# Optimization experiments

Hardware: AMD Instinct MI355X
Metric: run time of the kernel (lower is better)

## Reference

```python
import jax, jax.numpy as jnp
import numpy as np

L, D, H, M = 4, 256, 8, 1024  # num_blocks, emb_dim, num_heads, mlp_dim
B, N = 8, 1024
HD = H * D  # per-head dim == emb_dim in this module (hidden_dims = emb_dim*num_heads)


def setup_inputs() -> dict:
    key = jax.random.key(0)
    ks = jax.random.split(key, 6)
    s = 0.02
    return {
        "x": jax.random.normal(ks[0], (B, N, D), jnp.float32),
        "ln1_g": jnp.ones((L, D), jnp.float32),
        "ln1_b": jnp.zeros((L, D), jnp.float32),
        "qkv_w": jax.random.normal(ks[1], (L, D, 3 * HD), jnp.float32) * s,
        "qkv_b": jnp.zeros((L, 3 * HD), jnp.float32),
        "proj_w": jax.random.normal(ks[2], (L, HD, D), jnp.float32) * s,
        "proj_b": jnp.zeros((L, D), jnp.float32),
        "ln2_g": jnp.ones((L, D), jnp.float32),
        "ln2_b": jnp.zeros((L, D), jnp.float32),
        "w1": jax.random.normal(ks[3], (L, D, M), jnp.float32) * s,
        "b1": jnp.zeros((L, M), jnp.float32),
        "w2": jax.random.normal(ks[4], (L, M, D), jnp.float32) * s,
        "b2": jnp.zeros((L, D), jnp.float32),
    }


def _layernorm(x, g, b):
    m = x.mean(-1, keepdims=True)
    v = x.var(-1, keepdims=True)  # torch LayerNorm: biased variance, eps=1e-5
    return (x - m) * jax.lax.rsqrt(v + 1e-5) * g + b


def reference(x, ln1_g, ln1_b, qkv_w, qkv_b, proj_w, proj_b, ln2_g, ln2_b, w1, b1, w2, b2):
    b, n, d = x.shape
    scale = d ** 0.5  # source intends emb_dim**0.5; NOTE: applied AFTER softmax (bug preserved)
    for i in range(L):
        # --- attention residual block (pre-norm) ---
        h = _layernorm(x, ln1_g[i], ln1_b[i])
        qkv = (h @ qkv_w[i] + qkv_b[i]).reshape(b, n, H, d, 3)  # 'b n (h d qkv)'
        q = jnp.transpose(qkv[..., 0], (0, 2, 1, 3))  # [b,H,n,d]
        k = jnp.transpose(qkv[..., 1], (0, 2, 1, 3))
        v = jnp.transpose(qkv[..., 2], (0, 2, 1, 3))
        energy = jnp.einsum('bhqd,bhkd->bhqk', q, k)
        attn = jax.nn.softmax(energy, axis=-1) / scale  # post-softmax scaling as in source
        o = jnp.einsum('bhal,bhlv->bhav', attn, v)
        o = jnp.transpose(o, (0, 2, 1, 3)).reshape(b, n, H * d)
        x = x + (o @ proj_w[i] + proj_b[i])
        # --- MLP residual block (pre-norm) ---
        h = _layernorm(x, ln2_g[i], ln2_b[i])
        h = jax.nn.gelu(h @ w1[i] + b1[i], approximate=False)  # torch nn.GELU default = exact
        x = x + (h @ w2[i] + b2[i])
    return x
```

## Files before the change

kernel.cpp:

```cpp
#include <hip/hip_runtime.h>
#include <cstdint>
#include <cmath>

typedef float f32x4 __attribute__((ext_vector_type(4)));
typedef short s16x8 __attribute__((ext_vector_type(8)));

__device__ __forceinline__ unsigned short f2bf(float f) {
  union { float f; unsigned u; } v; v.f = f;
  unsigned r = v.u + 0x7FFFu + ((v.u >> 16) & 1u);
  return (unsigned short)(r >> 16);
}

__device__ __forceinline__ void async16(const void* g, void* l) {
  __builtin_amdgcn_global_load_lds(
      (const __attribute__((address_space(1))) unsigned int*)g,
      (__attribute__((address_space(3))) unsigned int*)l, 16, 0, 0);
}

#define MFMA(a,b,c) __builtin_amdgcn_mfma_f32_16x16x32_bf16((a),(b),(c),0,0,0)

#define Lb 4
#define Dm 256
#define Hh 8
#define Mm 1024
#define Bb 8
#define Nn 1024
#define ROWS (Bb*Nn)
#define QKVN (3*Hh*Dm)

__global__ __launch_bounds__(256) void ln_kernel(const float* __restrict__ x,
                                                 const float* __restrict__ g,
                                                 const float* __restrict__ b,
                                                 unsigned short* __restrict__ out) {
  int wave = threadIdx.x >> 6, lane = threadIdx.x & 63;
  int row = blockIdx.x * 4 + wave;
  const float4* xr = (const float4*)(x + (size_t)row * Dm);
  float4 v = xr[lane];
  float s = v.x + v.y + v.z + v.w;
  float s2 = v.x*v.x + v.y*v.y + v.z*v.z + v.w*v.w;
  #pragma unroll
  for (int off = 1; off < 64; off <<= 1) {
    s  += __shfl_xor(s,  off);
    s2 += __shfl_xor(s2, off);
  }
  float mean = s * (1.0f/Dm);
  float var  = s2 * (1.0f/Dm) - mean*mean;
  float inv  = rsqrtf(var + 1e-5f);
  float4 gg = ((const float4*)g)[lane];
  float4 bb = ((const float4*)b)[lane];
  ushort4 o;
  o.x = f2bf((v.x-mean)*inv*gg.x + bb.x);
  o.y = f2bf((v.y-mean)*inv*gg.y + bb.y);
  o.z = f2bf((v.z-mean)*inv*gg.z + bb.z);
  o.w = f2bf((v.w-mean)*inv*gg.w + bb.w);
  ((ushort4*)(out + (size_t)row * Dm))[lane] = o;
}

__global__ __launch_bounds__(256) void lncomb_kernel(const float* __restrict__ xin,
                                                     const float* __restrict__ pp, int nz,
                                                     const float* __restrict__ g,
                                                     const float* __restrict__ b,
                                                     float* __restrict__ xout,
                                                     unsigned short* __restrict__ hb) {
  int wave = threadIdx.x >> 6, lane = threadIdx.x & 63;
  int row = blockIdx.x * 4 + wave;
  size_t base = (size_t)row * Dm;
  float4 v = ((const float4*)(xin + base))[lane];
  #pragma unroll 4
  for (int z = 0; z < nz; z++) {
    float4 p = ((const float4*)(pp + (size_t)z * ROWS * Dm + base))[lane];
    v.x += p.x; v.y += p.y; v.z += p.z; v.w += p.w;
  }
  ((float4*)(xout + base))[lane] = v;
  float s = v.x + v.y + v.z + v.w;
  float s2 = v.x*v.x + v.y*v.y + v.z*v.z + v.w*v.w;
  #pragma unroll
  for (int off = 1; off < 64; off <<= 1) {
    s  += __shfl_xor(s,  off);
    s2 += __shfl_xor(s2, off);
  }
  float mean = s * (1.0f/Dm);
  float var  = s2 * (1.0f/Dm) - mean*mean;
  float inv  = rsqrtf(var + 1e-5f);
  float4 gg = ((const float4*)g)[lane];
  float4 bb = ((const float4*)b)[lane];
  ushort4 o;
  o.x = f2bf((v.x-mean)*inv*gg.x + bb.x);
  o.y = f2bf((v.y-mean)*inv*gg.y + bb.y);
  o.z = f2bf((v.z-mean)*inv*gg.z + bb.z);
  o.w = f2bf((v.w-mean)*inv*gg.w + bb.w);
  ((ushort4*)(hb + base))[lane] = o;
}

__global__ __launch_bounds__(256) void comb_out_kernel(const float* __restrict__ xin,
                                                       const float* __restrict__ pp, int nz,
                                                       float* __restrict__ out) {
  int wave = threadIdx.x >> 6, lane = threadIdx.x & 63;
  int row = blockIdx.x * 4 + wave;
  size_t base = (size_t)row * Dm;
  float4 v = ((const float4*)(xin + base))[lane];
  #pragma unroll 4
  for (int z = 0; z < nz; z++) {
    float4 p = ((const float4*)(pp + (size_t)z * ROWS * Dm + base))[lane];
    v.x += p.x; v.y += p.y; v.z += p.z; v.w += p.w;
  }
  ((float4*)(out + base))[lane] = v;
}

template<bool PERM>
__global__ __launch_bounds__(256) void convT(const float* __restrict__ w,
                                             unsigned short* __restrict__ wt,
                                             int Kd, int Nd) {
  __shared__ float tile[32][33];
  int nt = blockIdx.x * 32, kt = blockIdx.y * 32, l = blockIdx.z;
  int tx = threadIdx.x & 31, ty = threadIdx.x >> 5;
  const float* src = w + ((size_t)l * Kd + kt) * Nd + nt;
  #pragma unroll
  for (int r = 0; r < 4; r++)
    tile[ty + r*8][tx] = src[(size_t)(ty + r*8) * Nd + tx];
  __syncthreads();
  #pragma unroll
  for (int r = 0; r < 4; r++) {
    int nl = ty + r*8;
    int j = nt + nl;
    int n = j;
    if (PERM) {
      int hh = j / 768, rem = j - hh*768;
      int dd = rem / 3, c = rem - dd*3;
      n = c*2048 + hh*256 + dd;
    }
    wt[((size_t)l * Nd + n) * Kd + kt + tx] = f2bf(tile[tx][nl]);
  }
}

__global__ void conv_bias(const float* __restrict__ bsrc, float* __restrict__ bperm) {
  int i = blockIdx.x * 256 + threadIdx.x;
  int l = i / QKVN, n = i - l*QKVN;
  int c = n >> 11, hh = (n >> 8) & 7, dd = n & 255;
  bperm[i] = bsrc[l*QKVN + hh*768 + dd*3 + c];
}

template<int EPI>
__global__ __launch_bounds__(256, 2) void gemm_bt(const unsigned short* __restrict__ A,
                                                  const unsigned short* __restrict__ Bt,
                                                  const float* __restrict__ bias,
                                                  void* __restrict__ outv,
                                                  unsigned short* __restrict__ vtg,
                                                  int M, int N, int Kstride, int Ksub) {
  constexpr int BM = 128, BN = 128, BK = 32;
  __shared__ __align__(16) unsigned short As[2][BM * BK];
  __shared__ __align__(16) unsigned short Bs[2][BN * BK];
  __shared__ __align__(16) unsigned short vtile[(EPI == 3) ? 128 * 136 : 1];
  int tid = threadIdx.x;
  int lane = tid & 63, wave = tid >> 6;
  int wm = (wave >> 1) * 64, wn = (wave & 1) * 64;
  int mblk = blockIdx.y * BM, nblk = blockIdx.x * BN;
  int l15 = lane & 15, q4 = lane >> 4;

  f32x4 acc[4][4] = {};

  int r0 = tid >> 2;
  int ch = (tid & 3) ^ ((tid >> 3) & 3);
  const unsigned short* Ag = A + (size_t)blockIdx.z * Ksub
                               + (size_t)(mblk + r0) * Kstride + ch*8;
  const unsigned short* Bg = Bt + (size_t)blockIdx.z * Ksub
                               + (size_t)(nblk + r0) * Kstride + ch*8;

  async16(Ag,                      As[0] + tid*8);
  async16(Ag + (size_t)64*Kstride, As[0] + 2048 + tid*8);
  async16(Bg,                      Bs[0] + tid*8);
  async16(Bg + (size_t)64*Kstride, Bs[0] + 2048 + tid*8);

  int xsw = (q4 ^ ((l15 >> 1) & 3)) * 8;

  int nk = Ksub / BK;
  for (int i = 0; i < nk; i++) {
    __syncthreads();
    if (i + 1 < nk) {
      int k0 = (i + 1) * BK;
      unsigned short* Asl = As[(i+1)&1] + tid*8;
      unsigned short* Bsl = Bs[(i+1)&1] + tid*8;
      async16(Ag + k0,                      Asl);
      async16(Ag + (size_t)64*Kstride + k0, Asl + 2048);
      async16(Bg + k0,                      Bsl);
      async16(Bg + (size_t)64*Kstride + k0, Bsl + 2048);
    }
    const unsigned short* Ac = As[i&1];
    const unsigned short* Bc = Bs[i&1];
    s16x8 af[4], bf[4];
    #pragma unroll
    for (int j = 0; j < 4; j++)
      af[j] = *(const s16x8*)(Ac + (wm + j*16 + l15) * BK + xsw);
    #pragma unroll
    for (int j = 0; j < 4; j++)
      bf[j] = *(const s16x8*)(Bc + (wn + j*16 + l15) * BK + xsw);
    #pragma unroll
    for (int mi = 0; mi < 4; mi++)
      #pragma unroll
      for (int ni = 0; ni < 4; ni++)
        acc[mi][ni] = MFMA(af[mi], bf[ni], acc[mi][ni]);
  }

  auto scalar_epi = [&]() {
    #pragma unroll
    for (int mi = 0; mi < 4; mi++)
      #pragma unroll
      for (int ni = 0; ni < 4; ni++) {
        int col = nblk + wn + ni*16 + l15;
        float bcol;
        if (EPI == 4) bcol = (blockIdx.z == 0) ? bias[col] : 0.0f;
        else          bcol = bias[col];
        #pragma unroll
        for (int r = 0; r < 4; r++) {
          int row = mblk + wm + mi*16 + q4*4 + r;
          float v = acc[mi][ni][r] + bcol;
          if (EPI == 1) {
            v = 0.5f * v * (1.0f + erff(v * 0.70710678118f));
            ((unsigned short*)outv)[(size_t)row * N + col] = f2bf(v);
          } else if (EPI == 3) {
            ((unsigned short*)outv)[(size_t)row * 4096 + col] = f2bf(v);
          } else if (EPI == 4) {
            float* out = (float*)outv + (size_t)blockIdx.z * M * N;
            out[(size_t)row * N + col] = v;
          }
        }
      }
  };

  if constexpr (EPI == 3) {
    if (nblk >= 4096) {
      #pragma unroll
      for (int mi = 0; mi < 4; mi++)
        #pragma unroll
        for (int ni = 0; ni < 4; ni++) {
          int col_l = wn + ni*16 + l15;
          float bcol = bias[nblk + col_l];
          int seq_l = wm + mi*16 + q4*4;
          ushort4 pk4;
          pk4.x = f2bf(acc[mi][ni][0] + bcol);
          pk4.y = f2bf(acc[mi][ni][1] + bcol);
          pk4.z = f2bf(acc[mi][ni][2] + bcol);
          pk4.w = f2bf(acc[mi][ni][3] + bcol);
          *(ushort4*)(vtile + col_l * 136 + seq_l) = pk4;
        }
      __syncthreads();
      int base = nblk - 4096;
      int hh = base >> 8, ddb = base & 255;
      int bi = mblk >> 10, n0 = mblk & 1023;
      unsigned short* dst = vtg + ((size_t)(bi*8 + hh) * 256 + ddb) * 1024 + n0;
      #pragma unroll
      for (int p = 0; p < 8; p++) {
        int flat = p * 2048 + tid * 8;
        int ddl = flat >> 7, ns = flat & 127;
        int4 v4 = *(const int4*)(vtile + ddl * 136 + ns);
        *(int4*)(dst + (size_t)ddl * 1024 + ns) = v4;
      }
    } else {
      scalar_epi();
    }
  } else {
    scalar_epi();
  }
}

__global__ __launch_bounds__(256, 2) void attn_kernel(const unsigned short* __restrict__ qk,
                                                      const unsigned short* __restrict__ vt,
                                                      unsigned short* __restrict__ obuf) {
  int bh = blockIdx.x;
  int b = bh >> 3, h = bh & 7;
  int qt = blockIdx.y;
  int tid = threadIdx.x, lane = tid & 63, wave = tid >> 6;
  int l15 = lane & 15, q4 = lane >> 4;

  __shared__ __align__(16) unsigned short Ks[2][32 * 256];
  __shared__ __align__(16) unsigned short Vs[2][256 * 32];

  const unsigned short* Qb  = qk + (size_t)(b * Nn) * 4096 + h * 256;
  const unsigned short* Kb  = Qb + 2048;
  const unsigned short* VTb = vt + (size_t)bh * 256 * 1024;

  int qbase = qt * 128 + wave * 32;

  s16x8 qf[2][8];
  #pragma unroll
  for (int s = 0; s < 2; s++) {
    const unsigned short* qp = Qb + (size_t)(qbase + s*16 + l15) * 4096 + q4*8;
    #pragma unroll
    for (int c = 0; c < 8; c++) qf[s][c] = *(const s16x8*)(qp + c*32);
  }

  f32x4 oacc[2][16] = {};
  float lrun[2] = {0.f, 0.f};

  int ke[4], kc_[4], ve_[4];
  #pragma unroll
  for (int ii = 0; ii < 4; ii++) {
    int s = tid + ii*256;
    ke[ii] = s * 8;
    int kyr = s >> 5, kch = (s & 31) ^ (kyr & 7);
    kc_[ii] = kyr * 4096 + kch * 8;
    int vr = s >> 2, vch = (s & 3) ^ ((s >> 3) & 3);
    ve_[ii] = vr * 1024 + vch * 8;
  }

  #pragma unroll
  for (int ii = 0; ii < 4; ii++) {
    async16(Kb + kc_[ii],  Ks[0] + ke[ii]);
    async16(VTb + ve_[ii], Vs[0] + ke[ii]);
  }

  int vsw = (q4 ^ ((l15 >> 1) & 3)) * 8;

  for (int kt = 0; kt < 32; kt++) {
    __syncthreads();
    if (kt + 1 < 32) {
      int buf = (kt + 1) & 1;
      #pragma unroll
      for (int ii = 0; ii < 4; ii++) {
        async16(Kb + (size_t)(kt+1)*32*4096 + kc_[ii], Ks[buf] + ke[ii]);
        async16(VTb + (kt+1)*32 + ve_[ii],             Vs[buf] + ke[ii]);
      }
    }
    const unsigned short* Kc = Ks[kt & 1];
    const unsigned short* Vc = Vs[kt & 1];

    f32x4 sacc[2][2] = {};
    #pragma unroll
    for (int c = 0; c < 8; c++)
      #pragma unroll
      for (int mb = 0; mb < 2; mb++) {
        s16x8 af = *(const s16x8*)(Kc + (mb*16 + l15)*256 + (((c*4 + q4) ^ (l15 & 7)))*8);
        sacc[0][mb] = MFMA(af, qf[0][c], sacc[0][mb]);
        sacc[1][mb] = MFMA(af, qf[1][c], sacc[1][mb]);
      }

    int pk[2][2][2];
    #pragma unroll
    for (int s = 0; s < 2; s++) {
      float v0[4], v1[4];
      float rs = 0.f;
      #pragma unroll
      for (int r = 0; r < 4; r++) {
        v0[r] = __expf(sacc[s][0][r] - 12.0f);
        v1[r] = __expf(sacc[s][1][r] - 12.0f);
        rs += v0[r] + v1[r];
      }
      rs += __shfl_xor(rs, 16);
      rs += __shfl_xor(rs, 32);
      lrun[s] += rs;
      pk[s][0][0] = (int)f2bf(v0[0]) | ((int)f2bf(v0[1]) << 16);
      pk[s][0][1] = (int)f2bf(v0[2]) | ((int)f2bf(v0[3]) << 16);
      pk[s][1][0] = (int)f2bf(v1[0]) | ((int)f2bf(v1[1]) << 16);
      pk[s][1][1] = (int)f2bf(v1[2]) | ((int)f2bf(v1[3]) << 16);
    }

    int src0 = l15 + 16 * ((q4 & 1) * 2);
    int src1 = src0 + 16;
    bool sel = (q4 < 2);
    s16x8 pa[2];
    #pragma unroll
    for (int s = 0; s < 2; s++) {
      int u00 = __shfl(pk[s][0][0], src0), u10 = __shfl(pk[s][1][0], src0);
      int u01 = __shfl(pk[s][0][1], src0), u11 = __shfl(pk[s][1][1], src0);
      int u02 = __shfl(pk[s][0][0], src1), u12 = __shfl(pk[s][1][0], src1);
      int u03 = __shfl(pk[s][0][1], src1), u13 = __shfl(pk[s][1][1], src1);
      union { int u[4]; s16x8 v; } P;
      P.u[0] = sel ? u00 : u10;
      P.u[1] = sel ? u01 : u11;
      P.u[2] = sel ? u02 : u12;
      P.u[3] = sel ? u03 : u13;
      pa[s] = P.v;
    }

    #pragma unroll
    for (int nb = 0; nb < 16; nb++) {
      s16x8 vf = *(const s16x8*)(Vc + (nb*16 + l15)*32 + vsw);
      oacc[0][nb] = MFMA(pa[0], vf, oacc[0][nb]);
      oacc[1][nb] = MFMA(pa[1], vf, oacc[1][nb]);
    }
  }

  #pragma unroll
  for (int s = 0; s < 2; s++) {
    float lr[4];
    #pragma unroll
    for (int r = 0; r < 4; r++) lr[r] = __shfl(lrun[s], q4*4 + r);
    #pragma unroll
    for (int r = 0; r < 4; r++) {
      float sc = 1.0f / (lr[r] * 16.0f);
      int row = b * Nn + qbase + s*16 + q4*4 + r;
      unsigned short* op = obuf + (size_t)row * 2048 + h * 256;
      #pragma unroll
      for (int nb = 0; nb < 16; nb++)
        op[nb*16 + l15] = f2bf(oacc[s][nb][r] * sc);
    }
  }
}

extern "C" void kernel_launch(void* const* d_in, const int* in_sizes, int n_in,
                              void* d_out, int out_size, void* d_ws, size_t ws_size,
                              hipStream_t stream) {
  const float* x_in   = (const float*)d_in[0];
  const float* ln1_g  = (const float*)d_in[1];
  const float* ln1_b  = (const float*)d_in[2];
  const float* qkv_w  = (const float*)d_in[3];
  const float* qkv_b  = (const float*)d_in[4];
  const float* proj_w = (const float*)d_in[5];
  const float* proj_b = (const float*)d_in[6];
  const float* ln2_g  = (const float*)d_in[7];
  const float* ln2_b  = (const float*)d_in[8];
  const float* w1     = (const float*)d_in[9];
  const float* b1     = (const float*)d_in[10];
  const float* w2     = (const float*)d_in[11];
  const float* b2     = (const float*)d_in[12];

  char* ws = (char*)d_ws;
  size_t off = 0;
  float*          X0   = (float*)(ws + off);          off += (size_t)ROWS*Dm*4;
  unsigned short* Hb   = (unsigned short*)(ws + off); off += (size_t)ROWS*Dm*2;
  char*           QKre = ws + off;                    off += (size_t)ROWS*4096*2;
  unsigned short* VT   = (unsigned short*)(ws + off); off += (size_t)64*256*1024*2;
  unsigned short* O    = (unsigned short*)(ws + off); off += (size_t)ROWS*2048*2;
  unsigned short* H1   = (unsigned short*)(ws + off); off += (size_t)ROWS*Mm*2;
  unsigned short* QKVW = (unsigned short*)(ws + off); off += (size_t)Lb*QKVN*Dm*2;
  float*          QKVB = (float*)(ws + off);          off += (size_t)Lb*QKVN*4;
  unsigned short* PRJW = (unsigned short*)(ws + off); off += (size_t)Lb*Dm*2048*2;
  unsigned short* W1T  = (unsigned short*)(ws + off); off += (size_t)Lb*Mm*Dm*2;
  unsigned short* W2T  = (unsigned short*)(ws + off); off += (size_t)Lb*Dm*Mm*2;

  unsigned short* QK = (unsigned short*)QKre;
  float*          PP = (float*)QKre;
  float*          X1 = (float*)(QKre + (size_t)36*1024*1024);

  hipMemcpyAsync(X0, x_in, (size_t)ROWS*Dm*4, hipMemcpyDeviceToDevice, stream);

  convT<true><<<dim3(QKVN/32, Dm/32, Lb), 256, 0, stream>>>(qkv_w, QKVW, Dm, QKVN);
  conv_bias<<<Lb*QKVN/256, 256, 0, stream>>>(qkv_b, QKVB);
  convT<false><<<dim3(Dm/32, 2048/32, Lb), 256, 0, stream>>>(proj_w, PRJW, 2048, Dm);
  convT<false><<<dim3(Mm/32, Dm/32, Lb), 256, 0, stream>>>(w1, W1T, Dm, Mm);
  convT<false><<<dim3(Dm/32, Mm/32, Lb), 256, 0, stream>>>(w2, W2T, Mm, Dm);

  for (int l = 0; l < Lb; l++) {
    if (l == 0)
      ln_kernel<<<ROWS/4, 256, 0, stream>>>(X0, ln1_g, ln1_b, Hb);
    gemm_bt<3><<<dim3(QKVN/128, ROWS/128), 256, 0, stream>>>(
        Hb, QKVW + (size_t)l*QKVN*Dm, QKVB + (size_t)l*QKVN, QK, VT,
        ROWS, QKVN, Dm, Dm);
    attn_kernel<<<dim3(Bb*Hh, Nn/128), 256, 0, stream>>>(QK, VT, O);
    gemm_bt<4><<<dim3(Dm/128, ROWS/128, 4), 256, 0, stream>>>(
        O, PRJW + (size_t)l*Dm*2048, proj_b + l*Dm, PP, nullptr,
        ROWS, Dm, 2048, 512);
    lncomb_kernel<<<ROWS/4, 256, 0, stream>>>(X0, PP, 4, ln2_g + l*Dm, ln2_b + l*Dm,
                                              X1, Hb);
    gemm_bt<1><<<dim3(Mm/128, ROWS/128), 256, 0, stream>>>(
        Hb, W1T + (size_t)l*Mm*Dm, b1 + l*Mm, H1, nullptr, ROWS, Mm, Dm, Dm);
    gemm_bt<4><<<dim3(Dm/128, ROWS/128, 2), 256, 0, stream>>>(
        H1, W2T + (size_t)l*Dm*Mm, b2 + l*Dm, PP, nullptr,
        ROWS, Dm, Mm, 512);
    if (l < Lb - 1) {
      lncomb_kernel<<<ROWS/4, 256, 0, stream>>>(X1, PP, 2, ln1_g + (l+1)*Dm,
                                                ln1_b + (l+1)*Dm, X0, Hb);
    } else {
      comb_out_kernel<<<ROWS/4, 256, 0, stream>>>(X1, PP, 2, (float*)d_out);
    }
  }
}
```

Measured before the change: 935.4 us.

## Load K and V fragments directly from global memory in attention kernel

Removes the double-buffered LDS staging of K and V tiles (async global-to-LDS copies plus per-tile __syncthreads) and has each wave read its MFMA operand fragments straight from global memory. This eliminates block-wide barriers and LDS traffic and frees LDS, which may allow higher occupancy. In exchange, the four waves of a block each fetch the same K/V data independently, relying on L1/L2 cache hits, and the loads are no longer overlapped with compute through explicit prefetch, so latency may be exposed.

```diff
diff --git a/kernel.cpp b/kernel.cpp
--- a/kernel.cpp
+++ b/kernel.cpp
@@ -272,9 +272,6 @@
   int tid = threadIdx.x, lane = tid & 63, wave = tid >> 6;
   int l15 = lane & 15, q4 = lane >> 4;
 
-  __shared__ __align__(16) unsigned short Ks[2][32 * 256];
-  __shared__ __align__(16) unsigned short Vs[2][256 * 32];
-
   const unsigned short* Qb  = qk + (size_t)(b * Nn) * 4096 + h * 256;
   const unsigned short* Kb  = Qb + 2048;
   const unsigned short* VTb = vt + (size_t)bh * 256 * 1024;
@@ -292,44 +289,17 @@
   f32x4 oacc[2][16] = {};
   float lrun[2] = {0.f, 0.f};
 
-  int ke[4], kc_[4], ve_[4];
-  #pragma unroll
-  for (int ii = 0; ii < 4; ii++) {
-    int s = tid + ii*256;
-    ke[ii] = s * 8;
-    int kyr = s >> 5, kch = (s & 31) ^ (kyr & 7);
-    kc_[ii] = kyr * 4096 + kch * 8;
-    int vr = s >> 2, vch = (s & 3) ^ ((s >> 3) & 3);
-    ve_[ii] = vr * 1024 + vch * 8;
-  }
-
-  #pragma unroll
-  for (int ii = 0; ii < 4; ii++) {
-    async16(Kb + kc_[ii],  Ks[0] + ke[ii]);
-    async16(VTb + ve_[ii], Vs[0] + ke[ii]);
-  }
-
-  int vsw = (q4 ^ ((l15 >> 1) & 3)) * 8;
+  const unsigned short* Kl = Kb + (size_t)l15 * 4096 + q4*8;
+  const unsigned short* Vl = VTb + (size_t)l15 * 1024 + q4*8;
 
   for (int kt = 0; kt < 32; kt++) {
-    __syncthreads();
-    if (kt + 1 < 32) {
-      int buf = (kt + 1) & 1;
-      #pragma unroll
-      for (int ii = 0; ii < 4; ii++) {
-        async16(Kb + (size_t)(kt+1)*32*4096 + kc_[ii], Ks[buf] + ke[ii]);
-        async16(VTb + (kt+1)*32 + ve_[ii],             Vs[buf] + ke[ii]);
-      }
-    }
-    const unsigned short* Kc = Ks[kt & 1];
-    const unsigned short* Vc = Vs[kt & 1];
-
+    const unsigned short* Kp = Kl + (size_t)kt * 32 * 4096;
     f32x4 sacc[2][2] = {};
     #pragma unroll
     for (int c = 0; c < 8; c++)
       #pragma unroll
       for (int mb = 0; mb < 2; mb++) {
-        s16x8 af = *(const s16x8*)(Kc + (mb*16 + l15)*256 + (((c*4 + q4) ^ (l15 & 7)))*8);
+        s16x8 af = *(const s16x8*)(Kp + (size_t)mb*16*4096 + c*32);
         sacc[0][mb] = MFMA(af, qf[0][c], sacc[0][mb]);
         sacc[1][mb] = MFMA(af, qf[1][c], sacc[1][mb]);
       }
@@ -372,9 +342,10 @@
       pa[s] = P.v;
     }
 
+    const unsigned short* Vp = Vl + kt * 32;
     #pragma unroll
     for (int nb = 0; nb < 16; nb++) {
-      s16x8 vf = *(const s16x8*)(Vc + (nb*16 + l15)*32 + vsw);
+      s16x8 vf = *(const s16x8*)(Vp + (size_t)nb*16*1024);
       oacc[0][nb] = MFMA(pa[0], vf, oacc[0][nb]);
       oacc[1][nb] = MFMA(pa[1], vf, oacc[1][nb]);
     }
```

Result: slower. 1.734 ms (+85.4%).
